# Performance work log

Measured on AMD Instinct MI355X. Metric: run time of the kernel, lower is better.

Reference implementation:

```python
import jax, jax.numpy as jnp
import numpy as np

B, S, D = 1, 2304, 3072
H, HD = 24, 128
COND = 256          # (256//8)*(256//8)*16//64
N_LORAS = 1
BLOCK = S - COND * N_LORAS
RANK = 128
ALPHA = 128.0
LORA_W = 1.0
IP_SCALE = 1.0
T_IP, D_IP = 128, 4096
EPS = 1e-5


def setup_inputs() -> dict:
    key = jax.random.key(0)
    ks = jax.random.split(key, 24)
    r = lambda i, shape, s=0.02: jax.random.normal(ks[i], shape, dtype=jnp.float32) * s
    inp = {
        'hidden_states': jax.random.normal(ks[0], (B, S, D), dtype=jnp.float32),
        'image_emb': jax.random.normal(ks[1], (B, T_IP, D_IP), dtype=jnp.float32),
        'rope_cos': jax.random.uniform(ks[2], (S, HD), dtype=jnp.float32),
        'rope_sin': jax.random.uniform(ks[3], (S, HD), dtype=jnp.float32),
        'Wq': r(4, (D, D)), 'bq': jnp.zeros((D,), jnp.float32),
        'Wk': r(5, (D, D)), 'bk': jnp.zeros((D,), jnp.float32),
        'Wv': r(6, (D, D)), 'bv': jnp.zeros((D,), jnp.float32),
        'q_down': r(7, (RANK, D), 1.0 / RANK), 'q_up': r(8, (D, RANK)),
        'k_down': r(9, (RANK, D), 1.0 / RANK), 'k_up': r(10, (D, RANK)),
        'v_down': r(11, (RANK, D), 1.0 / RANK), 'v_up': r(12, (D, RANK)),
        'norm_q_w': jnp.ones((HD,), jnp.float32),
        'norm_k_w': jnp.ones((HD,), jnp.float32),
        'Wk_ip': r(13, (D, D_IP)),
        'Wv_ip': r(14, (D, D_IP)),
    }
    return inp


def _rmsnorm(x, w=None):
    v = jnp.mean(x * x, axis=-1, keepdims=True)
    y = x * jax.lax.rsqrt(v + EPS)
    return y * w if w is not None else y


def _rope(x, cos, sin):
    # diffusers apply_rotary_emb, use_real=True, unbind_dim=-1 (interleaved pairs)
    xp = x.reshape(*x.shape[:-1], HD // 2, 2)
    x_rot = jnp.stack([-xp[..., 1], xp[..., 0]], axis=-1).reshape(x.shape)
    return x * cos[None, None] + x_rot * sin[None, None]


def _lora(x, down, up, tok_mask):
    h = x * tok_mask[None, :, None]
    return (h @ down.T) @ up.T * (ALPHA / RANK)


def _forward(hidden_states, Wq, bq, Wk, bk, Wv, bv,
             q_down, q_up, k_down, k_up, v_down, v_up,
             norm_q_w, norm_k_w, rope_cos, rope_sin,
             Wk_ip, Wv_ip, image_emb):
    x = hidden_states
    idx = jnp.arange(S)
    # LoRA #0 token mask: only the cond-token rows are nonzero
    tok_mask = ((idx >= BLOCK) & (idx < BLOCK + COND)).astype(x.dtype)

    q = x @ Wq.T + bq + LORA_W * _lora(x, q_down, q_up, tok_mask)
    k = x @ Wk.T + bk + LORA_W * _lora(x, k_down, k_up, tok_mask)
    v = x @ Wv.T + bv + LORA_W * _lora(x, v_down, v_up, tok_mask)

    # [B,S,D] -> [B,H,S,HD]
    to_heads = lambda t: t.reshape(B, S, H, HD).transpose(0, 2, 1, 3)
    q, k, v = to_heads(q), to_heads(k), to_heads(v)

    q = _rmsnorm(q, norm_q_w)
    k = _rmsnorm(k, norm_k_w)
    q = _rope(q, rope_cos, rope_sin)
    k = _rope(k, rope_cos, rope_sin)

    # block-causal mask: main rows attend everywhere; each cond block attends only to itself
    row, col = idx[:, None], idx[None, :]
    same_blk = (row >= BLOCK) & (col >= BLOCK) & ((row - BLOCK) // COND == (col - BLOCK) // COND)
    bias = jnp.where((row < BLOCK) | same_blk, 0.0, -1e20).astype(q.dtype)

    scale = 1.0 / jnp.sqrt(jnp.asarray(HD, q.dtype))
    logits = jnp.einsum('bhqd,bhkd->bhqk', q, k) * scale + bias
    p = jax.nn.softmax(logits, axis=-1)
    out = jnp.einsum('bhqk,bhkd->bhqd', p, v)
    hs = out.transpose(0, 2, 1, 3).reshape(B, S, D)

    # IP-adapter branch
    k_ip = (image_emb @ Wk_ip.T).reshape(B, T_IP, H, HD).transpose(0, 2, 1, 3)
    v_ip = (image_emb @ Wv_ip.T).reshape(B, T_IP, H, HD).transpose(0, 2, 1, 3)
    k_ip = _rmsnorm(k_ip)
    ip_logits = jnp.einsum('bhqd,bhkd->bhqk', q, k_ip) * scale
    ip_out = jnp.einsum('bhqk,bhkd->bhqd', jax.nn.softmax(ip_logits, axis=-1), v_ip)
    ip_hs = ip_out.transpose(0, 2, 1, 3).reshape(B, S, D)
    hs = hs + IP_SCALE * ip_hs
    return hs


def reference(hidden_states, image_emb, rope_cos, rope_sin, Wq, bq, Wk, bk, Wv, bv,
              q_down, q_up, k_down, k_up, v_down, v_up, norm_q_w, norm_k_w, Wk_ip, Wv_ip):
    hs = _forward(hidden_states, Wq, bq, Wk, bk, Wv, bv,
                  q_down, q_up, k_down, k_up, v_down, v_up,
                  norm_q_w, norm_k_w, rope_cos, rope_sin, Wk_ip, Wv_ip, image_emb)
    # use_cond=True split
    return hs[:, :BLOCK, :], hs[:, BLOCK:, :]
```

## Files before the change

### kernel.cpp

```cpp
#include <hip/hip_runtime.h>

#define S_TOT 2304
#define D_TOT 3072
#define NH    24
#define HD    128
#define BLK_R 2048
#define TIP   128
#define DIP   4096
#define KS    3

typedef __attribute__((ext_vector_type(4))) float f4;
typedef __attribute__((ext_vector_type(8))) short bh8;
typedef unsigned short u16;
typedef unsigned int   u32;
typedef unsigned long long u64;

__device__ __forceinline__ u16 f2bf(float f) {
    u32 u = __float_as_uint(f);
    u32 r = (u + 0x7fffu + ((u >> 16) & 1u)) >> 16;
    return (u16)r;
}
__device__ __forceinline__ uint4 pack8u(float4 a, float4 b) {
    uint4 u;
    u.x = (u32)f2bf(a.x) | ((u32)f2bf(a.y) << 16);
    u.y = (u32)f2bf(a.z) | ((u32)f2bf(a.w) << 16);
    u.z = (u32)f2bf(b.x) | ((u32)f2bf(b.y) << 16);
    u.w = (u32)f2bf(b.z) | ((u32)f2bf(b.w) << 16);
    return u;
}
__device__ __forceinline__ bh8 pack8v(float4 a, float4 b) {
    bh8 v;
    v[0] = (short)f2bf(a.x); v[1] = (short)f2bf(a.y);
    v[2] = (short)f2bf(a.z); v[3] = (short)f2bf(a.w);
    v[4] = (short)f2bf(b.x); v[5] = (short)f2bf(b.y);
    v[6] = (short)f2bf(b.z); v[7] = (short)f2bf(b.w);
    return v;
}

__device__ __forceinline__ void gemm_body(const float* __restrict__ A, const float* __restrict__ B,
                                          const float* __restrict__ bias, float* __restrict__ C,
                                          int M, int N, int K, int mode, int kbeg, int kend,
                                          u16* As, u16* Bs)
{
    const int tid  = threadIdx.x;
    const int wv   = tid >> 6;
    const int lane = tid & 63;
    const int quad = lane >> 4;
    const int l16  = lane & 15;
    const int wm   = (wv >> 1) << 6;
    const int wn   = (wv & 1) << 6;
    const int m0   = blockIdx.x << 7;
    const int n0   = blockIdx.y << 7;

    f4 acc[4][4] = {};

    for (int k0 = kbeg; k0 < kend; k0 += 64) {
#pragma unroll
        for (int p = 0; p < 4; ++p) {
            int idx = (p << 11) + (tid << 3);
            int r = idx >> 6, c = idx & 63;
            const float* ap = A + (size_t)(m0 + r) * K + k0 + c;
            *(uint4*)(&As[idx]) = pack8u(*(const float4*)ap, *(const float4*)(ap + 4));
            const float* bp = B + (size_t)(n0 + r) * K + k0 + c;
            *(uint4*)(&Bs[idx]) = pack8u(*(const float4*)bp, *(const float4*)(bp + 4));
        }
        __syncthreads();
#pragma unroll
        for (int kk = 0; kk < 2; ++kk) {
            bh8 a[4], b[4];
#pragma unroll
            for (int i = 0; i < 4; ++i)
                a[i] = *(const bh8*)(&As[(wm + (i << 4) + l16) * 64 + (kk << 5) + (quad << 3)]);
#pragma unroll
            for (int i = 0; i < 4; ++i)
                b[i] = *(const bh8*)(&Bs[(wn + (i << 4) + l16) * 64 + (kk << 5) + (quad << 3)]);
#pragma unroll
            for (int mt = 0; mt < 4; ++mt)
#pragma unroll
                for (int nt = 0; nt < 4; ++nt)
                    acc[mt][nt] = __builtin_amdgcn_mfma_f32_16x16x32_bf16(a[mt], b[nt], acc[mt][nt], 0, 0, 0);
        }
        __syncthreads();
    }
#pragma unroll
    for (int mt = 0; mt < 4; ++mt) {
#pragma unroll
        for (int nt = 0; nt < 4; ++nt) {
            int n = n0 + wn + (nt << 4) + l16;
            float bs = bias ? bias[n] : 0.0f;
#pragma unroll
            for (int r = 0; r < 4; ++r) {
                int m = m0 + wm + (mt << 4) + (quad << 2) + r;
                size_t o = (size_t)m * N + n;
                float v = acc[mt][nt][r] + bs;
                if (mode == 0)      C[o] = v;
                else if (mode == 1) C[o] += v;
                else                atomicAdd(&C[o], v);
            }
        }
    }
}

__global__ __launch_bounds__(256)
void gemm_qkv_k(const float* __restrict__ x,
                const float* __restrict__ Wq, const float* __restrict__ bq, float* __restrict__ qf,
                const float* __restrict__ Wk, const float* __restrict__ bk, float* __restrict__ kf,
                const float* __restrict__ Wv, const float* __restrict__ bv, float* __restrict__ vf)
{
    __shared__ u16 As[128 * 64];
    __shared__ u16 Bs[128 * 64];
    int z = blockIdx.z;
    const float* B  = z == 0 ? Wq : (z == 1 ? Wk : Wv);
    const float* bi = z == 0 ? bq : (z == 1 ? bk : bv);
    float*       C  = z == 0 ? qf : (z == 1 ? kf : vf);
    gemm_body(x, B, bi, C, S_TOT, D_TOT, D_TOT, 0, 0, D_TOT, As, Bs);
}

__global__ __launch_bounds__(256)
void gemm_loraup_k(const float* __restrict__ t1,
                   const float* __restrict__ qup, const float* __restrict__ kup, const float* __restrict__ vup,
                   float* __restrict__ qf, float* __restrict__ kf, float* __restrict__ vf)
{
    __shared__ u16 As[128 * 64];
    __shared__ u16 Bs[128 * 64];
    int z = blockIdx.z;
    const float* A = t1 + (size_t)z * 32768;
    const float* B = z == 0 ? qup : (z == 1 ? kup : vup);
    float*       C = (z == 0 ? qf : (z == 1 ? kf : vf)) + (size_t)BLK_R * D_TOT;
    gemm_body(A, B, nullptr, C, 256, D_TOT, 128, 1, 0, 128, As, Bs);
}

__global__ __launch_bounds__(256)
void gemm_ip_k(const float* __restrict__ img,
               const float* __restrict__ Wkip, const float* __restrict__ Wvip,
               float* __restrict__ kipf, float* __restrict__ vipf)
{
    __shared__ u16 As[128 * 64];
    __shared__ u16 Bs[128 * 64];
    int z = blockIdx.z;
    int sel = z >> 3, cz = z & 7;
    const float* B = sel ? Wvip : Wkip;
    float*       C = sel ? vipf : kipf;
    gemm_body(img, B, nullptr, C, TIP, D_TOT, DIP, 2, cz * 512, cz * 512 + 512, As, Bs);
}

__global__ __launch_bounds__(256)
void lora_down_k(const float* __restrict__ X,
                 const float* __restrict__ qdn, const float* __restrict__ kdn, const float* __restrict__ vdn,
                 float* __restrict__ t1)
{
    int y = blockIdx.y;
    const float* Dwn = y == 0 ? qdn : (y == 1 ? kdn : vdn);
    float* T1 = t1 + (size_t)y * 32768;
    int wv = threadIdx.x >> 6, lane = threadIdx.x & 63;
    int quad = lane >> 4, l16 = lane & 15;
    int gw = blockIdx.x * 4 + wv;
    int mt = gw >> 3, nt = gw & 7;
    const float* ap = X + (size_t)(BLK_R + (mt << 4) + l16) * D_TOT + (quad << 3);
    const float* bp = Dwn + (size_t)((nt << 4) + l16) * D_TOT + (quad << 3);
    f4 acc = {};
    for (int c = 0; c < 96; ++c) {
        bh8 a = pack8v(*(const float4*)(ap + (c << 5)), *(const float4*)(ap + (c << 5) + 4));
        bh8 b = pack8v(*(const float4*)(bp + (c << 5)), *(const float4*)(bp + (c << 5) + 4));
        acc = __builtin_amdgcn_mfma_f32_16x16x32_bf16(a, b, acc, 0, 0, 0);
    }
#pragma unroll
    for (int r = 0; r < 4; ++r) {
        int s  = (mt << 4) + (quad << 2) + r;
        int rr = (nt << 4) + l16;
        T1[(size_t)s * 128 + rr] = acc[r];
    }
}

template <int ROPE>
__device__ __forceinline__ void norm_rope_body(const float* __restrict__ X, const float* __restrict__ w,
                                               const float* __restrict__ ct, const float* __restrict__ st,
                                               u16* __restrict__ Out, int Slen, float omul, int g, int lane)
{
    int s = g / NH, h = g % NH;
    const float* xp = X + (size_t)s * D_TOT + (h << 7) + (lane << 1);
    float2 xv = *(const float2*)xp;
    float ss = xv.x * xv.x + xv.y * xv.y;
#pragma unroll
    for (int off = 1; off <= 32; off <<= 1) ss += __shfl_xor(ss, off);
    float invr = rsqrtf(ss * (1.0f / 128.0f) + 1e-5f);
    float a = xv.x * invr, b = xv.y * invr;
    if (w) { a *= w[lane << 1]; b *= w[(lane << 1) + 1]; }
    float o0 = a, o1 = b;
    if (ROPE) {
        float c0 = ct[(size_t)s * HD + (lane << 1)], c1 = ct[(size_t)s * HD + (lane << 1) + 1];
        float n0 = st[(size_t)s * HD + (lane << 1)], n1 = st[(size_t)s * HD + (lane << 1) + 1];
        o0 = a * c0 - b * n0;
        o1 = b * c1 + a * n1;
    }
    o0 *= omul; o1 *= omul;
    size_t oo = ((size_t)h * Slen + s) * HD + (lane << 1);
    u32 pack = (u32)f2bf(o0) | ((u32)f2bf(o1) << 16);
    *(u32*)(&Out[oo]) = pack;
}

__global__ __launch_bounds__(256)
void norm_qk_k(const float* __restrict__ qf, const float* __restrict__ kf,
               const float* __restrict__ nqw, const float* __restrict__ nkw,
               const float* __restrict__ ct, const float* __restrict__ st,
               u16* __restrict__ Qb, u16* __restrict__ Kb, float qscale)
{
    int g = blockIdx.x * 4 + (threadIdx.x >> 6);
    int lane = threadIdx.x & 63;
    if (blockIdx.y == 0)
        norm_rope_body<1>(qf, nqw, ct, st, Qb, S_TOT, qscale, g, lane);
    else
        norm_rope_body<1>(kf, nkw, ct, st, Kb, S_TOT, 1.0f, g, lane);
}

__global__ __launch_bounds__(256)
void norm_ip_k(const float* __restrict__ X, u16* __restrict__ Out)
{
    int g = blockIdx.x * 4 + (threadIdx.x >> 6);
    int lane = threadIdx.x & 63;
    norm_rope_body<0>(X, nullptr, nullptr, nullptr, Out, TIP, 1.0f, g, lane);
}

__global__ __launch_bounds__(256)
void transpose_v_k(const float* __restrict__ V, u16* __restrict__ Vt, int Slen)
{
    __shared__ u16 tile[64][130];
    int h = blockIdx.y;
    int s0 = blockIdx.x << 6;
    int tid = threadIdx.x;
#pragma unroll
    for (int p = 0; p < 32; ++p) {
        int flat = (p << 8) + tid;
        int si = flat >> 7, d = flat & 127;
        tile[si][d] = f2bf(V[(size_t)(s0 + si) * D_TOT + (h << 7) + d]);
    }
    __syncthreads();
#pragma unroll
    for (int p = 0; p < 32; ++p) {
        int flat = (p << 8) + tid;
        int d = flat >> 6, si = flat & 63;
        Vt[((size_t)(h << 7) + d) * Slen + s0 + si] = tile[si][d];
    }
}

__global__ __launch_bounds__(256)
void attn_k(const u16* __restrict__ Qb, const u16* __restrict__ Kb,
            const u16* __restrict__ Vt, float* __restrict__ Out,
            float* __restrict__ Opart, float2* __restrict__ Ml,
            int Lk, int cond_start, int per, int mode, int nqt, int nblk)
{
    __shared__ __align__(16) u16 Ks[2][32 * 136];
    __shared__ __align__(16) u16 Vs[2][128 * 40];
    __shared__ __align__(16) u16 Pl[4][16 * 40];

    const int bid = blockIdx.x;
    const int f = (bid & 7) * (nblk >> 3) + (bid >> 3);
    const int qt = f % nqt;
    const int h  = (f / nqt) % NH;
    const int ch = f / (nqt * NH);

    const int tid = threadIdx.x;
    const int wv = tid >> 6;
    const int lane = tid & 63;
    const int quad = lane >> 4, l16 = lane & 15;
    const int sb = (qt << 6) + (wv << 4);

    bh8 qf[4];
    const u16* qp = Qb + ((size_t)h * S_TOT + sb + l16) * HD + (quad << 3);
#pragma unroll
    for (int c = 0; c < 4; ++c) qf[c] = *(const bh8*)(qp + (c << 5));

    f4 o[8] = {};
    float mrow[4]  = {-1e30f, -1e30f, -1e30f, -1e30f};
    float lpart[4] = {0.f, 0.f, 0.f, 0.f};
    u16* pl = &Pl[wv][0];

    const int kt0 = (sb >= BLK_R) ? cond_start : 0;
    const int ktN = Lk >> 5;
    int kt_lo = ch * per;       if (kt0 > kt_lo) kt_lo = kt0;
    int kt_hi = ch * per + per; if (ktN < kt_hi) kt_hi = ktN;

    if (kt_lo < kt_hi) {
        const int rowK = tid >> 3, colK = (tid & 7) << 4;
        const int rowV = tid >> 1, colV = (tid & 1) << 4;
        const u16* ksrc0 = Kb + ((size_t)h * Lk + rowK) * HD + colK;
        const u16* vsrc0 = Vt + (((size_t)h << 7) + rowV) * Lk + colV;
        u16* kdst = &Ks[0][0] + rowK * 136 + colK;
        u16* vdst = &Vs[0][0] + rowV * 40 + colV;

        {
            const u16* ks = ksrc0 + ((size_t)kt_lo << 5) * HD;
            const u16* vs = vsrc0 + ((size_t)kt_lo << 5);
            uint4 a = *(const uint4*)ks, b = *(const uint4*)(ks + 8);
            uint4 c = *(const uint4*)vs, d = *(const uint4*)(vs + 8);
            *(uint4*)kdst = a; *(uint4*)(kdst + 8) = b;
            *(uint4*)vdst = c; *(uint4*)(vdst + 8) = d;
        }
        __syncthreads();

        int p = 0;
        for (int kt = kt_lo; kt < kt_hi; ++kt) {
            uint4 pk0 = {}, pk1 = {}, pv0 = {}, pv1 = {};
            const bool pf = (kt + 1 < kt_hi);
            if (pf) {
                const u16* ks = ksrc0 + ((size_t)(kt + 1) << 5) * HD;
                const u16* vs = vsrc0 + ((size_t)(kt + 1) << 5);
                pk0 = *(const uint4*)ks; pk1 = *(const uint4*)(ks + 8);
                pv0 = *(const uint4*)vs; pv1 = *(const uint4*)(vs + 8);
            }
            const u16* kb = &Ks[p][0];
            const u16* vb = &Vs[p][0];

            f4 s0 = {}, s1 = {};
            __builtin_amdgcn_s_setprio(1);
#pragma unroll
            for (int c = 0; c < 4; ++c) {
                bh8 k0 = *(const bh8*)(kb + l16 * 136 + (c << 5) + (quad << 3));
                bh8 k1 = *(const bh8*)(kb + (16 + l16) * 136 + (c << 5) + (quad << 3));
                s0 = __builtin_amdgcn_mfma_f32_16x16x32_bf16(qf[c], k0, s0, 0, 0, 0);
                s1 = __builtin_amdgcn_mfma_f32_16x16x32_bf16(qf[c], k1, s1, 0, 0, 0);
            }
            __builtin_amdgcn_s_setprio(0);

            float mx[4];
#pragma unroll
            for (int r = 0; r < 4; ++r) mx[r] = fmaxf(s0[r], s1[r]);
#pragma unroll
            for (int off = 1; off <= 8; off <<= 1)
#pragma unroll
                for (int r = 0; r < 4; ++r) mx[r] = fmaxf(mx[r], __shfl_xor(mx[r], off));

            int grow = 0;
#pragma unroll
            for (int r = 0; r < 4; ++r) grow |= (mx[r] > mrow[r]) ? 1 : 0;
            if (__any(grow)) {
#pragma unroll
                for (int r = 0; r < 4; ++r) {
                    float mn = fmaxf(mrow[r], mx[r]);
                    float al = exp2f(mrow[r] - mn);
                    mrow[r] = mn;
                    lpart[r] *= al;
#pragma unroll
                    for (int dt = 0; dt < 8; ++dt) o[dt][r] *= al;
                }
            }
            float p0[4], p1[4];
#pragma unroll
            for (int r = 0; r < 4; ++r) {
                p0[r] = exp2f(s0[r] - mrow[r]);
                p1[r] = exp2f(s1[r] - mrow[r]);
                lpart[r] += p0[r] + p1[r];
            }
#pragma unroll
            for (int r = 0; r < 4; ++r) {
                pl[((quad << 2) + r) * 40 + l16]      = f2bf(p0[r]);
                pl[((quad << 2) + r) * 40 + 16 + l16] = f2bf(p1[r]);
            }
            bh8 pa = *(const bh8*)(pl + l16 * 40 + (quad << 3));
            __builtin_amdgcn_s_setprio(1);
#pragma unroll
            for (int dt = 0; dt < 8; ++dt) {
                bh8 v = *(const bh8*)(vb + ((dt << 4) + l16) * 40 + (quad << 3));
                o[dt] = __builtin_amdgcn_mfma_f32_16x16x32_bf16(pa, v, o[dt], 0, 0, 0);
            }
            __builtin_amdgcn_s_setprio(0);

            if (pf) {
                u16* kd = kdst + (p ^ 1) * (32 * 136);
                u16* vd = vdst + (p ^ 1) * (128 * 40);
                *(uint4*)kd = pk0; *(uint4*)(kd + 8) = pk1;
                *(uint4*)vd = pv0; *(uint4*)(vd + 8) = pv1;
            }
            __syncthreads();
            p ^= 1;
        }
    }

#pragma unroll
    for (int off = 1; off <= 8; off <<= 1)
#pragma unroll
        for (int r = 0; r < 4; ++r) lpart[r] += __shfl_xor(lpart[r], off);

    if (mode == 0) {
        float inv[4];
#pragma unroll
        for (int r = 0; r < 4; ++r) inv[r] = 1.0f / lpart[r];
#pragma unroll
        for (int dt = 0; dt < 8; ++dt) {
#pragma unroll
            for (int r = 0; r < 4; ++r) {
                int row = sb + (quad << 2) + r;
                int col = (h << 7) + (dt << 4) + l16;
                Out[(size_t)row * D_TOT + col] = o[dt][r] * inv[r];
            }
        }
    } else {
        const size_t cb = ((size_t)ch * NH + h) * S_TOT;
#pragma unroll
        for (int dt = 0; dt < 8; ++dt) {
#pragma unroll
            for (int r = 0; r < 4; ++r) {
                int row = sb + (quad << 2) + r;
                Opart[(cb + row) * 128 + (dt << 4) + l16] = o[dt][r];
            }
        }
        if (l16 == 0) {
#pragma unroll
            for (int r = 0; r < 4; ++r) {
                int row = sb + (quad << 2) + r;
                Ml[cb + row] = (float2){mrow[r], lpart[r]};
            }
        }
    }
}

__global__ __launch_bounds__(256)
void merge_k(const float* __restrict__ Opart, const float2* __restrict__ Ml,
             const float* __restrict__ ipo, float* __restrict__ Out)
{
    int g = blockIdx.x * 4 + (threadIdx.x >> 6);
    int lane = threadIdx.x & 63;
    int h = g / S_TOT;
    int s = g - h * S_TOT;
    float m[KS], l[KS];
#pragma unroll
    for (int c = 0; c < KS; ++c) {
        float2 ml = Ml[((size_t)c * NH + h) * S_TOT + s];
        m[c] = ml.x; l[c] = ml.y;
    }
    float M = m[0];
#pragma unroll
    for (int c = 1; c < KS; ++c) M = fmaxf(M, m[c]);
    float w[KS], lt = 0.f;
#pragma unroll
    for (int c = 0; c < KS; ++c) { w[c] = exp2f(m[c] - M); lt += w[c] * l[c]; }
    float inv = 1.0f / lt;
    float ax = 0.f, ay = 0.f;
#pragma unroll
    for (int c = 0; c < KS; ++c) {
        const float2 ov = *(const float2*)&Opart[(((size_t)c * NH + h) * S_TOT + s) * 128 + (lane << 1)];
        ax += w[c] * ov.x; ay += w[c] * ov.y;
    }
    size_t oidx = (size_t)s * D_TOT + (h << 7) + (lane << 1);
    float2 ip = *(const float2*)&ipo[oidx];
    float2 res = {ax * inv + ip.x, ay * inv + ip.y};
    *(float2*)&Out[oidx] = res;
}

static const u64 B_OP   = 0;
static const u64 B_QF   = 0;
static const u64 B_KF   = 28311552;
static const u64 B_VF   = 56623104;
static const u64 B_KIPF = 84934656;
static const u64 B_VIPF = 86507520;
static const u64 B_T1   = 88080384;
static const u64 B_QB   = 88473600;
static const u64 B_KB   = 102629376;
static const u64 B_VT   = 116785152;
static const u64 B_KIPB = 130940928;
static const u64 B_VIPT = 131727360;
static const u64 B_ML   = 132513792;
static const u64 B_IPO  = 134217728;

extern "C" void kernel_launch(void* const* d_in, const int* in_sizes, int n_in,
                              void* d_out, int out_size, void* d_ws, size_t ws_size,
                              hipStream_t stream) {
    (void)in_sizes; (void)n_in; (void)out_size; (void)ws_size;
    const float* x    = (const float*)d_in[0];
    const float* img  = (const float*)d_in[1];
    const float* rc   = (const float*)d_in[2];
    const float* rsn  = (const float*)d_in[3];
    const float* Wq   = (const float*)d_in[4];
    const float* bq   = (const float*)d_in[5];
    const float* Wk   = (const float*)d_in[6];
    const float* bk   = (const float*)d_in[7];
    const float* Wv   = (const float*)d_in[8];
    const float* bv   = (const float*)d_in[9];
    const float* qdn  = (const float*)d_in[10];
    const float* qup  = (const float*)d_in[11];
    const float* kdn  = (const float*)d_in[12];
    const float* kup  = (const float*)d_in[13];
    const float* vdn  = (const float*)d_in[14];
    const float* vup  = (const float*)d_in[15];
    const float* nqw  = (const float*)d_in[16];
    const float* nkw  = (const float*)d_in[17];
    const float* Wkip = (const float*)d_in[18];
    const float* Wvip = (const float*)d_in[19];

    float*  qf   = (float*)((char*)d_ws + B_QF);
    float*  kf   = (float*)((char*)d_ws + B_KF);
    float*  vf   = (float*)((char*)d_ws + B_VF);
    float*  kipf = (float*)((char*)d_ws + B_KIPF);
    float*  vipf = (float*)((char*)d_ws + B_VIPF);
    float*  t1   = (float*)((char*)d_ws + B_T1);
    u16*    Qb   = (u16*)((char*)d_ws + B_QB);
    u16*    Kb   = (u16*)((char*)d_ws + B_KB);
    u16*    Vt   = (u16*)((char*)d_ws + B_VT);
    u16*    Kipb = (u16*)((char*)d_ws + B_KIPB);
    u16*    Vipt = (u16*)((char*)d_ws + B_VIPT);
    float*  opart= (float*)((char*)d_ws + B_OP);
    float2* ml   = (float2*)((char*)d_ws + B_ML);
    float*  ipo  = (float*)((char*)d_ws + B_IPO);
    float*  outf = (float*)d_out;

    const float QSCALE = 0.08838834764831845f * 1.4426950408889634f;

    hipMemsetAsync((char*)d_ws + B_KIPF, 0, 2 * 1572864, stream);

    gemm_qkv_k<<<dim3(18, 24, 3), dim3(256), 0, stream>>>(x, Wq, bq, qf, Wk, bk, kf, Wv, bv, vf);

    lora_down_k<<<dim3(32, 3), dim3(256), 0, stream>>>(x, qdn, kdn, vdn, t1);
    gemm_loraup_k<<<dim3(2, 24, 3), dim3(256), 0, stream>>>(t1, qup, kup, vup, qf, kf, vf);

    gemm_ip_k<<<dim3(1, 24, 16), dim3(256), 0, stream>>>(img, Wkip, Wvip, kipf, vipf);

    norm_qk_k<<<dim3(13824, 2), dim3(256), 0, stream>>>(qf, kf, nqw, nkw, rc, rsn, Qb, Kb, QSCALE);
    norm_ip_k<<<dim3(768), dim3(256), 0, stream>>>(kipf, Kipb);
    transpose_v_k<<<dim3(36, 24), dim3(256), 0, stream>>>(vf, Vt, S_TOT);
    transpose_v_k<<<dim3(2, 24),  dim3(256), 0, stream>>>(vipf, Vipt, TIP);

    attn_k<<<dim3(2592), dim3(256), 0, stream>>>(Qb, Kb, Vt, nullptr, opart, ml, S_TOT, 64, 24, 1, 36, 2592);
    attn_k<<<dim3(864),  dim3(256), 0, stream>>>(Qb, Kipb, Vipt, ipo, nullptr, nullptr, TIP, 0, 4, 0, 36, 864);
    merge_k<<<dim3(13824), dim3(256), 0, stream>>>(opart, ml, ipo, outf);
}
```

Before: 972.7 us.

## Pre-convert QKV GEMM operands to bf16 and stream them directly into LDS

A new kernel converts the hidden states and the three projection weights from fp32 to bf16 into workspace once per call. The QKV GEMM then loads bf16 tiles straight from global memory into LDS with global_load_lds, so it no longer converts fp32 tile by tile, which every block repeated. The LoRA-down kernel also reads the bf16 copy of x. In exchange there is an extra pass over the weights each call and about 56 MB of bf16 weights in workspace, overlapping buffers that are only written later.

```diff
diff --git a/kernel.cpp b/kernel.cpp
--- a/kernel.cpp
+++ b/kernel.cpp
@@ -37,11 +37,37 @@
     return v;
 }
 
-__device__ __forceinline__ void gemm_body(const float* __restrict__ A, const float* __restrict__ B,
-                                          const float* __restrict__ bias, float* __restrict__ C,
-                                          int M, int N, int K, int mode, int kbeg, int kend,
-                                          u16* As, u16* Bs)
-{
+__global__ __launch_bounds__(256)
+void conv_bf16_k(const float* __restrict__ s0, u16* __restrict__ d0, int n0c,
+                 const float* __restrict__ s1, u16* __restrict__ d1,
+                 const float* __restrict__ s2, u16* __restrict__ d2,
+                 const float* __restrict__ s3, u16* __restrict__ d3, int n1c)
+{
+    int y = blockIdx.y;
+    const float* s = y == 0 ? s0 : (y == 1 ? s1 : (y == 2 ? s2 : s3));
+    u16*         d = y == 0 ? d0 : (y == 1 ? d1 : (y == 2 ? d2 : d3));
+    int n = (y == 0) ? n0c : n1c;
+    int stride = gridDim.x * blockDim.x;
+    for (int i = blockIdx.x * blockDim.x + threadIdx.x; i < n; i += stride) {
+        float4 a = *(const float4*)(s + (size_t)i * 8);
+        float4 b = *(const float4*)(s + (size_t)i * 8 + 4);
+        *(uint4*)(d + (size_t)i * 8) = pack8u(a, b);
+    }
+}
+
+__global__ __launch_bounds__(256)
+void gemm_qkv_bf16_k(const u16* __restrict__ xb, const u16* __restrict__ Wb,
+                     const float* __restrict__ bq, const float* __restrict__ bk,
+                     const float* __restrict__ bv,
+                     float* __restrict__ qf, float* __restrict__ kf, float* __restrict__ vf)
+{
+    __shared__ __align__(16) u16 As[128 * 64];
+    __shared__ __align__(16) u16 Bs[128 * 64];
+    const int z = blockIdx.z;
+    const u16* Bw = Wb + (size_t)z * D_TOT * D_TOT;
+    const float* bias = z == 0 ? bq : (z == 1 ? bk : bv);
+    float* C = z == 0 ? qf : (z == 1 ? kf : vf);
+
     const int tid  = threadIdx.x;
     const int wv   = tid >> 6;
     const int lane = tid & 63;
@@ -52,6 +78,73 @@
     const int m0   = blockIdx.x << 7;
     const int n0   = blockIdx.y << 7;
 
+    const int srow = lane >> 3;
+    const int scol = (lane & 7) << 3;
+
+    f4 acc[4][4] = {};
+
+    for (int k0 = 0; k0 < D_TOT; k0 += 64) {
+#pragma unroll
+        for (int j = 0; j < 4; ++j) {
+            int seg = (j << 2) + wv;
+            int r = (seg << 3) + srow;
+            const u16* ga = xb + (size_t)(m0 + r) * D_TOT + k0 + scol;
+            const u16* gb = Bw + (size_t)(n0 + r) * D_TOT + k0 + scol;
+            __builtin_amdgcn_global_load_lds((const __attribute__((address_space(1))) void*)ga,
+                                             (__attribute__((address_space(3))) void*)(&As[seg << 9]),
+                                             16, 0, 0);
+            __builtin_amdgcn_global_load_lds((const __attribute__((address_space(1))) void*)gb,
+                                             (__attribute__((address_space(3))) void*)(&Bs[seg << 9]),
+                                             16, 0, 0);
+        }
+        __syncthreads();
+#pragma unroll
+        for (int kk = 0; kk < 2; ++kk) {
+            bh8 a[4], b[4];
+#pragma unroll
+            for (int i = 0; i < 4; ++i)
+                a[i] = *(const bh8*)(&As[(wm + (i << 4) + l16) * 64 + (kk << 5) + (quad << 3)]);
+#pragma unroll
+            for (int i = 0; i < 4; ++i)
+                b[i] = *(const bh8*)(&Bs[(wn + (i << 4) + l16) * 64 + (kk << 5) + (quad << 3)]);
+#pragma unroll
+            for (int mt = 0; mt < 4; ++mt)
+#pragma unroll
+                for (int nt = 0; nt < 4; ++nt)
+                    acc[mt][nt] = __builtin_amdgcn_mfma_f32_16x16x32_bf16(a[mt], b[nt], acc[mt][nt], 0, 0, 0);
+        }
+        __syncthreads();
+    }
+#pragma unroll
+    for (int mt = 0; mt < 4; ++mt) {
+#pragma unroll
+        for (int nt = 0; nt < 4; ++nt) {
+            int n = n0 + wn + (nt << 4) + l16;
+            float bs = bias[n];
+#pragma unroll
+            for (int r = 0; r < 4; ++r) {
+                int m = m0 + wm + (mt << 4) + (quad << 2) + r;
+                C[(size_t)m * D_TOT + n] = acc[mt][nt][r] + bs;
+            }
+        }
+    }
+}
+
+__device__ __forceinline__ void gemm_body(const float* __restrict__ A, const float* __restrict__ B,
+                                          const float* __restrict__ bias, float* __restrict__ C,
+                                          int M, int N, int K, int mode, int kbeg, int kend,
+                                          u16* As, u16* Bs)
+{
+    const int tid  = threadIdx.x;
+    const int wv   = tid >> 6;
+    const int lane = tid & 63;
+    const int quad = lane >> 4;
+    const int l16  = lane & 15;
+    const int wm   = (wv >> 1) << 6;
+    const int wn   = (wv & 1) << 6;
+    const int m0   = blockIdx.x << 7;
+    const int n0   = blockIdx.y << 7;
+
     f4 acc[4][4] = {};
 
     for (int k0 = kbeg; k0 < kend; k0 += 64) {
@@ -102,21 +195,6 @@
 }
 
 __global__ __launch_bounds__(256)
-void gemm_qkv_k(const float* __restrict__ x,
-                const float* __restrict__ Wq, const float* __restrict__ bq, float* __restrict__ qf,
-                const float* __restrict__ Wk, const float* __restrict__ bk, float* __restrict__ kf,
-                const float* __restrict__ Wv, const float* __restrict__ bv, float* __restrict__ vf)
-{
-    __shared__ u16 As[128 * 64];
-    __shared__ u16 Bs[128 * 64];
-    int z = blockIdx.z;
-    const float* B  = z == 0 ? Wq : (z == 1 ? Wk : Wv);
-    const float* bi = z == 0 ? bq : (z == 1 ? bk : bv);
-    float*       C  = z == 0 ? qf : (z == 1 ? kf : vf);
-    gemm_body(x, B, bi, C, S_TOT, D_TOT, D_TOT, 0, 0, D_TOT, As, Bs);
-}
-
-__global__ __launch_bounds__(256)
 void gemm_loraup_k(const float* __restrict__ t1,
                    const float* __restrict__ qup, const float* __restrict__ kup, const float* __restrict__ vup,
                    float* __restrict__ qf, float* __restrict__ kf, float* __restrict__ vf)
@@ -145,7 +223,7 @@
 }
 
 __global__ __launch_bounds__(256)
-void lora_down_k(const float* __restrict__ X,
+void lora_down_k(const u16* __restrict__ Xb,
                  const float* __restrict__ qdn, const float* __restrict__ kdn, const float* __restrict__ vdn,
                  float* __restrict__ t1)
 {
@@ -156,11 +234,11 @@
     int quad = lane >> 4, l16 = lane & 15;
     int gw = blockIdx.x * 4 + wv;
     int mt = gw >> 3, nt = gw & 7;
-    const float* ap = X + (size_t)(BLK_R + (mt << 4) + l16) * D_TOT + (quad << 3);
+    const u16*   ap = Xb + (size_t)(BLK_R + (mt << 4) + l16) * D_TOT + (quad << 3);
     const float* bp = Dwn + (size_t)((nt << 4) + l16) * D_TOT + (quad << 3);
     f4 acc = {};
     for (int c = 0; c < 96; ++c) {
-        bh8 a = pack8v(*(const float4*)(ap + (c << 5)), *(const float4*)(ap + (c << 5) + 4));
+        bh8 a = *(const bh8*)(ap + (c << 5));
         bh8 b = pack8v(*(const float4*)(bp + (c << 5)), *(const float4*)(bp + (c << 5) + 4));
         acc = __builtin_amdgcn_mfma_f32_16x16x32_bf16(a, b, acc, 0, 0, 0);
     }
@@ -454,6 +532,8 @@
 static const u64 B_KIPF = 84934656;
 static const u64 B_VIPF = 86507520;
 static const u64 B_T1   = 88080384;
+static const u64 B_XB   = 88473600;
+static const u64 B_WB   = 102629376;
 static const u64 B_QB   = 88473600;
 static const u64 B_KB   = 102629376;
 static const u64 B_VT   = 116785152;
@@ -493,6 +573,8 @@
     float*  kipf = (float*)((char*)d_ws + B_KIPF);
     float*  vipf = (float*)((char*)d_ws + B_VIPF);
     float*  t1   = (float*)((char*)d_ws + B_T1);
+    u16*    xb   = (u16*)((char*)d_ws + B_XB);
+    u16*    Wb   = (u16*)((char*)d_ws + B_WB);
     u16*    Qb   = (u16*)((char*)d_ws + B_QB);
     u16*    Kb   = (u16*)((char*)d_ws + B_KB);
     u16*    Vt   = (u16*)((char*)d_ws + B_VT);
@@ -507,9 +589,13 @@
 
     hipMemsetAsync((char*)d_ws + B_KIPF, 0, 2 * 1572864, stream);
 
-    gemm_qkv_k<<<dim3(18, 24, 3), dim3(256), 0, stream>>>(x, Wq, bq, qf, Wk, bk, kf, Wv, bv, vf);
-
-    lora_down_k<<<dim3(32, 3), dim3(256), 0, stream>>>(x, qdn, kdn, vdn, t1);
+    conv_bf16_k<<<dim3(1152, 4), dim3(256), 0, stream>>>(
+        x, xb, 884736,
+        Wq, Wb, Wk, Wb + (size_t)D_TOT * D_TOT, Wv, Wb + 2 * (size_t)D_TOT * D_TOT, 1179648);
+
+    gemm_qkv_bf16_k<<<dim3(18, 24, 3), dim3(256), 0, stream>>>(xb, Wb, bq, bk, bv, qf, kf, vf);
+
+    lora_down_k<<<dim3(32, 3), dim3(256), 0, stream>>>(xb, qdn, kdn, vdn, t1);
     gemm_loraup_k<<<dim3(2, 24, 3), dim3(256), 0, stream>>>(t1, qup, kup, vup, qf, kf, vf);
 
     gemm_ip_k<<<dim3(1, 24, 16), dim3(256), 0, stream>>>(img, Wkip, Wvip, kipf, vipf);
```

Measured after the change: 801.6 us. 1.21x faster.
